# Kernel optimization log

Hardware: AMD Instinct MI355X
Metric: run time of the kernel (lower is better)

The kernel has to match this reference:

```python
import jax, jax.numpy as jnp
import numpy as np
from jax import lax

H = 2048      # d_inner
N = 8         # half of d_state (conjugate-pair complex modes)
B, L, D_MODEL = 4, 4096, 1024
D_CONV = 4


def setup_inputs() -> dict:
    key = jax.random.key(0)
    ks = jax.random.split(key, 10)
    hidden_states = jax.random.normal(ks[0], (B, L, D_MODEL), dtype=jnp.float32)
    W_in = jax.random.normal(ks[1], (2 * H, D_MODEL), dtype=jnp.float32) / np.sqrt(D_MODEL)
    conv_w = jax.random.normal(ks[2], (H, D_CONV), dtype=jnp.float32) / np.sqrt(D_CONV)
    conv_b = jax.random.normal(ks[3], (H,), dtype=jnp.float32) * 0.1
    # S4D params: dt ~ loguniform(1e-3, 1e-1); A = -0.5 + i*pi*n (legs-ish diag init)
    u = jax.random.uniform(ks[4], (H,), dtype=jnp.float32)
    log_dt = jnp.log(1e-3) + u * (jnp.log(1e-1) - jnp.log(1e-3))
    log_A_real = jnp.log(0.5 * jnp.ones((H, N), dtype=jnp.float32))
    A_imag = jnp.pi * jnp.broadcast_to(jnp.arange(N, dtype=jnp.float32), (H, N)).copy()
    C_re = jax.random.normal(ks[5], (H, N), dtype=jnp.float32)
    C_im = jax.random.normal(ks[6], (H, N), dtype=jnp.float32)
    D = jnp.ones((H,), dtype=jnp.float32)
    W_out = jax.random.normal(ks[7], (D_MODEL, H), dtype=jnp.float32) / np.sqrt(H)
    return dict(hidden_states=hidden_states, W_in=W_in, conv_w=conv_w, conv_b=conv_b,
                log_dt=log_dt, log_A_real=log_A_real, A_imag=A_imag,
                C_re=C_re, C_im=C_im, D=D, W_out=W_out)


def _s4d_kernel(log_dt, log_A_real, A_imag, C_re, C_im, L):
    # S4D (diagonal SSM) convolution kernel, ZOH-style discretization.
    dt = jnp.exp(log_dt)                       # (H,)
    A = -jnp.exp(log_A_real) + 1j * A_imag      # (H,N) complex
    C = C_re + 1j * C_im                        # (H,N)
    dtA = dt[:, None] * A                       # (H,N)
    Ct = C * (jnp.exp(dtA) - 1.0) / A           # (H,N)
    t = jnp.arange(L, dtype=jnp.float32)
    vand = jnp.exp(dtA[:, :, None] * t)         # (H,N,L) Vandermonde
    return 2.0 * jnp.einsum('hn,hnl->hl', Ct, vand).real  # (H,L)


def reference(hidden_states, W_in, conv_w, conv_b, log_dt, log_A_real, A_imag, C_re, C_im, D, W_out):
    B, L, _ = hidden_states.shape
    # in_proj (no bias): (B,L,D) -> (B, 2H, L)
    xz = jnp.einsum('bld,ed->bel', hidden_states, W_in)
    x, z = jnp.split(xz, 2, axis=1)             # each (B,H,L)
    # causal depthwise conv1d + SiLU
    w = conv_w.shape[-1]
    xp = jnp.pad(x, ((0, 0), (0, 0), (w - 1, 0)))
    x = lax.conv_general_dilated(xp, conv_w[:, None, :], (1,), 'VALID',
                                 dimension_numbers=('NCH', 'OIH', 'NCH'),
                                 feature_group_count=x.shape[1])
    x = jax.nn.silu(x + conv_b[None, :, None])
    # S4 FFT long convolution + D skip
    k = _s4d_kernel(log_dt, log_A_real, A_imag, C_re, C_im, L)  # (H,L)
    n = 2 * L
    y = jnp.fft.irfft(jnp.fft.rfft(x, n=n) * jnp.fft.rfft(k, n=n), n=n)[..., :L]
    y = y + x * D[None, :, None]
    # SiLU gate and out_proj
    y = y * jax.nn.silu(z)
    return jnp.einsum('bhl,dh->bld', y, W_out)
```

## Files before the change

kernel.cpp:

```cpp
#include <hip/hip_runtime.h>
#include <hip/hip_bf16.h>
#include <math.h>

#define H_DIM 2048
#define N_ST 8
#define B_SZ 4
#define L_SEQ 4096
#define DMODEL 1024
#define DCONV 4
#define CL 128
#define NC (L_SEQ / CL)

typedef __bf16 bf16x8 __attribute__((ext_vector_type(8)));
typedef __bf16 bf16x4 __attribute__((ext_vector_type(4)));
typedef float f32x4 __attribute__((ext_vector_type(4)));

typedef const unsigned int __attribute__((address_space(1)))* gptr_t;
typedef unsigned int __attribute__((address_space(3)))* lptr_t;

__device__ __forceinline__ void gl_lds16(const __bf16* g, __bf16* l) {
    __builtin_amdgcn_global_load_lds((gptr_t)g, (lptr_t)l, 16, 0, 0);
}

#define WS_XZ     0
#define WS_YTH    8388608
#define WS_YTL    12582912
#define WS_COEF   16777216
#define WS_STATES 16875520
#define WS_LOOK   17924096
#define WS_HH     18186240
#define WS_HL     20283392
#define WS_WIH    22380544
#define WS_WIL    24477696
#define WS_WOH    26574848
#define WS_WOL    27623424

__global__ __launch_bounds__(256) void cvt_split4(const float* __restrict__ s,
                                                  __bf16* __restrict__ h,
                                                  __bf16* __restrict__ l, int n4) {
    int i = blockIdx.x * 256 + threadIdx.x;
    if (i >= n4) return;
    float4 v = ((const float4*)s)[i];
    float vv[4] = {v.x, v.y, v.z, v.w};
    bf16x4 hv, lv;
#pragma unroll
    for (int j = 0; j < 4; ++j) {
        __bf16 hb = (__bf16)vv[j];
        hv[j] = hb;
        lv[j] = (__bf16)(vv[j] - (float)hb);
    }
    *(bf16x4*)&h[(size_t)i * 4] = hv;
    *(bf16x4*)&l[(size_t)i * 4] = lv;
}

__global__ void coef_kernel(const float* __restrict__ log_dt,
                            const float* __restrict__ log_A_real,
                            const float* __restrict__ A_imag,
                            const float* __restrict__ C_re,
                            const float* __restrict__ C_im,
                            float* __restrict__ coef) {
    int i = blockIdx.x * blockDim.x + threadIdx.x;
    if (i >= H_DIM * N_ST) return;
    int h = i >> 3;
    float dt = expf(log_dt[h]);
    float Ar = -expf(log_A_real[i]);
    float Ai = A_imag[i];
    float er = expf(dt * Ar);
    float ang = dt * Ai;
    float wr = er * cosf(ang);
    float wi = er * sinf(ang);
    float den = Ar * Ar + Ai * Ai;
    float qr = ((wr - 1.f) * Ar + wi * Ai) / den;
    float qi = (wi * Ar - (wr - 1.f) * Ai) / den;
    float Cr = C_re[i], Ci = C_im[i];
    float Ctr = Cr * qr - Ci * qi;
    float Cti = Cr * qi + Ci * qr;
    float eCL = expf((float)CL * dt * Ar);
    float aCL = (float)CL * dt * Ai;
    float pr = eCL * cosf(aCL);
    float pi = eCL * sinf(aCL);
    const int HN = H_DIM * N_ST;
    coef[i]          = wr;
    coef[HN + i]     = wi;
    coef[2 * HN + i] = Ctr;
    coef[3 * HN + i] = Cti;
    coef[4 * HN + i] = pr;
    coef[5 * HN + i] = pi;
}

__global__ __launch_bounds__(256, 2) void gemm_split(const __bf16* __restrict__ Ah,
                                                     const __bf16* __restrict__ Al,
                                                     const __bf16* __restrict__ Bh,
                                                     const __bf16* __restrict__ Bl,
                                                     float* __restrict__ C,
                                                     int K, int ldc) {
    __shared__ __bf16 sAh[2][4096], sAl[2][4096], sBh[2][4096], sBl[2][4096];
    const int tid = threadIdx.x;
    const int lane = tid & 63;
    const int wid = tid >> 6;
    const int wrw = wid >> 1, wcw = wid & 1;
    const int bm = blockIdx.y, bn = blockIdx.x;

    const int r = tid & 127;
    const int kbq8 = (tid >> 7) * 8;
    const size_t arow = (size_t)(bm * 128 + r) * K;
    const size_t brow = (size_t)(bn * 128 + r) * K;

    f32x4 acc[4][4];
#pragma unroll
    for (int m = 0; m < 4; ++m)
#pragma unroll
        for (int n = 0; n < 4; ++n) acc[m][n] = (f32x4){0.f, 0.f, 0.f, 0.f};

    const int kb = lane >> 4, rr = lane & 15;

    auto stage = [&](int b, int k0) {
#pragma unroll
        for (int q = 0; q < 2; ++q) {
            const int lo = q * 2048 + tid * 8;
            const size_t go = (size_t)k0 + q * 16 + kbq8;
            gl_lds16(Ah + arow + go, &sAh[b][lo]);
            gl_lds16(Al + arow + go, &sAl[b][lo]);
            gl_lds16(Bh + brow + go, &sBh[b][lo]);
            gl_lds16(Bl + brow + go, &sBl[b][lo]);
        }
    };

    const int nt = K >> 5;
    stage(0, 0);
    stage(1, 32);
    asm volatile("s_waitcnt vmcnt(8)" ::: "memory");
    __builtin_amdgcn_s_barrier();

    for (int t = 0; t < nt; ++t) {
        const int cur = t & 1;

        bf16x8 fAh[4], fAl[4], fBh[4], fBl[4];
#pragma unroll
        for (int m = 0; m < 4; ++m) {
            int off = kb * 1024 + (wrw * 64 + m * 16 + rr) * 8;
            fAh[m] = *(const bf16x8*)&sAh[cur][off];
            fAl[m] = *(const bf16x8*)&sAl[cur][off];
        }
#pragma unroll
        for (int n = 0; n < 4; ++n) {
            int off = kb * 1024 + (wcw * 64 + n * 16 + rr) * 8;
            fBh[n] = *(const bf16x8*)&sBh[cur][off];
            fBl[n] = *(const bf16x8*)&sBl[cur][off];
        }
        asm volatile("s_waitcnt lgkmcnt(0)" ::: "memory");
        __builtin_amdgcn_sched_barrier(0);
        __builtin_amdgcn_s_barrier();
        __builtin_amdgcn_sched_barrier(0);
        if (t + 2 < nt) stage(cur, (t + 2) << 5);
        __builtin_amdgcn_s_setprio(1);
#pragma unroll
        for (int m = 0; m < 4; ++m)
#pragma unroll
            for (int n = 0; n < 4; ++n) {
                acc[m][n] = __builtin_amdgcn_mfma_f32_16x16x32_bf16(fAh[m], fBh[n], acc[m][n], 0, 0, 0);
                acc[m][n] = __builtin_amdgcn_mfma_f32_16x16x32_bf16(fAh[m], fBl[n], acc[m][n], 0, 0, 0);
                acc[m][n] = __builtin_amdgcn_mfma_f32_16x16x32_bf16(fAl[m], fBh[n], acc[m][n], 0, 0, 0);
            }
        __builtin_amdgcn_s_setprio(0);
        if (t + 2 < nt) asm volatile("s_waitcnt vmcnt(8)" ::: "memory");
        else            asm volatile("s_waitcnt vmcnt(0)" ::: "memory");
        __builtin_amdgcn_s_barrier();
    }

    const int rq = lane >> 4;
#pragma unroll
    for (int m = 0; m < 4; ++m)
#pragma unroll
        for (int n = 0; n < 4; ++n) {
            int col = bn * 128 + wcw * 64 + n * 16 + rr;
            int row0 = bm * 128 + wrw * 64 + m * 16 + rq * 4;
#pragma unroll
            for (int j = 0; j < 4; ++j)
                C[(size_t)(row0 + j) * ldc + col] = acc[m][n][j];
        }
}

__global__ __launch_bounds__(256) void scan_phase1(const float* __restrict__ xz,
                                                   const float* __restrict__ coef,
                                                   const float* __restrict__ conv_w,
                                                   const float* __restrict__ conv_b,
                                                   float* __restrict__ states,
                                                   float* __restrict__ look) {
    int t = blockIdx.x * 256 + threadIdx.x;
    int c = t & (NC - 1);
    int h = t >> 5;

    const int HN = H_DIM * N_ST;
    float wr[N_ST], wi[N_ST];
#pragma unroll
    for (int n = 0; n < N_ST; ++n) {
        wr[n] = coef[h * N_ST + n];
        wi[n] = coef[HN + h * N_ST + n];
    }
    float cw0 = conv_w[h * 4 + 0], cw1 = conv_w[h * 4 + 1];
    float cw2 = conv_w[h * 4 + 2], cw3 = conv_w[h * 4 + 3];
    float cb = conv_b[h];

    const float* xrow = xz + (size_t)h * L_SEQ + c * CL;
    float x3 = 0.f, x2 = 0.f, x1 = 0.f;
    if (c > 0) {
        float4 p = *(const float4*)(xrow - 4);
        x3 = p.y; x2 = p.z; x1 = p.w;
    }
    *(float4*)(look + (size_t)t * 4) = make_float4(x3, x2, x1, 0.f);

    float sr[N_ST], si[N_ST];
#pragma unroll
    for (int n = 0; n < N_ST; ++n) { sr[n] = 0.f; si[n] = 0.f; }

    for (int j = 0; j < CL; j += 4) {
        float4 v = *(const float4*)(xrow + j);
        float xv[4] = {v.x, v.y, v.z, v.w};
#pragma unroll
        for (int k = 0; k < 4; ++k) {
            float u = cw0 * x3 + cw1 * x2 + cw2 * x1 + cw3 * xv[k] + cb;
            float xc = u / (1.f + __expf(-u));
            x3 = x2; x2 = x1; x1 = xv[k];
#pragma unroll
            for (int n = 0; n < N_ST; ++n) {
                float nr = wr[n] * sr[n] - wi[n] * si[n] + xc;
                float ni = wr[n] * si[n] + wi[n] * sr[n];
                sr[n] = nr; si[n] = ni;
            }
        }
    }
    float* st = states + (size_t)t * (N_ST * 2);
#pragma unroll
    for (int n = 0; n < N_ST; ++n) { st[2 * n] = sr[n]; st[2 * n + 1] = si[n]; }
}

__global__ __launch_bounds__(256) void scan_phase2(const float* __restrict__ coef,
                                                   float* __restrict__ states) {
    int h = blockIdx.x * 256 + threadIdx.x;
    if (h >= H_DIM) return;
    const int HN = H_DIM * N_ST;
    float pr[N_ST], pi[N_ST];
#pragma unroll
    for (int n = 0; n < N_ST; ++n) {
        pr[n] = coef[4 * HN + h * N_ST + n];
        pi[n] = coef[5 * HN + h * N_ST + n];
    }
    float sr[N_ST], si[N_ST];
#pragma unroll
    for (int n = 0; n < N_ST; ++n) { sr[n] = 0.f; si[n] = 0.f; }
    float* base = states + (size_t)h * NC * (N_ST * 2);
    for (int c = 0; c < NC; ++c) {
        float* st = base + c * (N_ST * 2);
#pragma unroll
        for (int n = 0; n < N_ST; ++n) {
            float lr = st[2 * n], li = st[2 * n + 1];
            st[2 * n] = sr[n]; st[2 * n + 1] = si[n];
            float nr = pr[n] * sr[n] - pi[n] * si[n] + lr;
            float ni = pr[n] * si[n] + pi[n] * sr[n] + li;
            sr[n] = nr; si[n] = ni;
        }
    }
}

__global__ __launch_bounds__(256) void scan_phase3(float* __restrict__ xz,
                                                   const float* __restrict__ coef,
                                                   const float* __restrict__ conv_w,
                                                   const float* __restrict__ conv_b,
                                                   const float* __restrict__ Dvec,
                                                   const float* __restrict__ states,
                                                   const float* __restrict__ look) {
    int t = blockIdx.x * 256 + threadIdx.x;
    int c = t & (NC - 1);
    int h = t >> 5;

    const int HN = H_DIM * N_ST;
    float wr[N_ST], wi[N_ST], Ctr[N_ST], Cti[N_ST];
#pragma unroll
    for (int n = 0; n < N_ST; ++n) {
        wr[n]  = coef[h * N_ST + n];
        wi[n]  = coef[HN + h * N_ST + n];
        Ctr[n] = coef[2 * HN + h * N_ST + n];
        Cti[n] = coef[3 * HN + h * N_ST + n];
    }
    float cw0 = conv_w[h * 4 + 0], cw1 = conv_w[h * 4 + 1];
    float cw2 = conv_w[h * 4 + 2], cw3 = conv_w[h * 4 + 3];
    float cb = conv_b[h];
    float Dh = Dvec[h];

    float* xrow = xz + (size_t)h * L_SEQ + c * CL;
    const float* zrow = xz + (size_t)(H_DIM + h) * L_SEQ + c * CL;

    float4 lk = *(const float4*)(look + (size_t)t * 4);
    float x3 = lk.x, x2 = lk.y, x1 = lk.z;

    const float* st = states + (size_t)t * (N_ST * 2);
    float sr[N_ST], si[N_ST];
#pragma unroll
    for (int n = 0; n < N_ST; ++n) { sr[n] = st[2 * n]; si[n] = st[2 * n + 1]; }

    for (int j = 0; j < CL; j += 4) {
        float4 v = *(const float4*)(xrow + j);
        float4 zv = *(const float4*)(zrow + j);
        float xv[4] = {v.x, v.y, v.z, v.w};
        float zz[4] = {zv.x, zv.y, zv.z, zv.w};
        float out[4];
#pragma unroll
        for (int k = 0; k < 4; ++k) {
            float u = cw0 * x3 + cw1 * x2 + cw2 * x1 + cw3 * xv[k] + cb;
            float xc = u / (1.f + __expf(-u));
            x3 = x2; x2 = x1; x1 = xv[k];
            float accy = 0.f;
#pragma unroll
            for (int n = 0; n < N_ST; ++n) {
                float nr = wr[n] * sr[n] - wi[n] * si[n] + xc;
                float ni = wr[n] * si[n] + wi[n] * sr[n];
                sr[n] = nr; si[n] = ni;
                accy += Ctr[n] * nr - Cti[n] * ni;
            }
            float yv = 2.f * accy + Dh * xc;
            float g = zz[k] / (1.f + __expf(-zz[k]));
            out[k] = yv * g;
        }
        *(float4*)(xrow + j) = make_float4(out[0], out[1], out[2], out[3]);
    }
}

__global__ __launch_bounds__(256) void transpose_split(const float* __restrict__ y,
                                                       __bf16* __restrict__ th,
                                                       __bf16* __restrict__ tl) {
    __shared__ float tile[64][65];
    const int l0 = blockIdx.x * 64, h0 = blockIdx.y * 64;
    const int tid = threadIdx.x;
    const int r = tid >> 4, c4 = (tid & 15) * 4;
#pragma unroll
    for (int p = 0; p < 4; ++p) {
        float4 v = *(const float4*)(y + (size_t)(h0 + r + p * 16) * L_SEQ + l0 + c4);
        tile[r + p * 16][c4 + 0] = v.x;
        tile[r + p * 16][c4 + 1] = v.y;
        tile[r + p * 16][c4 + 2] = v.z;
        tile[r + p * 16][c4 + 3] = v.w;
    }
    __syncthreads();
    const int l = tid >> 2, hb = (tid & 3) * 16;
    float vals[16];
#pragma unroll
    for (int j = 0; j < 16; ++j) vals[j] = tile[hb + j][l];
    bf16x8 hv0, hv1, lv0, lv1;
#pragma unroll
    for (int j = 0; j < 8; ++j) {
        __bf16 hbv = (__bf16)vals[j];
        hv0[j] = hbv;
        lv0[j] = (__bf16)(vals[j] - (float)hbv);
        __bf16 hbv2 = (__bf16)vals[j + 8];
        hv1[j] = hbv2;
        lv1[j] = (__bf16)(vals[j + 8] - (float)hbv2);
    }
    size_t base = (size_t)(l0 + l) * H_DIM + h0 + hb;
    *(bf16x8*)&th[base] = hv0;
    *(bf16x8*)&th[base + 8] = hv1;
    *(bf16x8*)&tl[base] = lv0;
    *(bf16x8*)&tl[base + 8] = lv1;
}

extern "C" void kernel_launch(void* const* d_in, const int* in_sizes, int n_in,
                              void* d_out, int out_size, void* d_ws, size_t ws_size,
                              hipStream_t stream) {
    const float* hid        = (const float*)d_in[0];
    const float* W_in       = (const float*)d_in[1];
    const float* conv_w     = (const float*)d_in[2];
    const float* conv_b     = (const float*)d_in[3];
    const float* log_dt     = (const float*)d_in[4];
    const float* log_A_real = (const float*)d_in[5];
    const float* A_imag     = (const float*)d_in[6];
    const float* C_re       = (const float*)d_in[7];
    const float* C_im       = (const float*)d_in[8];
    const float* Dv         = (const float*)d_in[9];
    const float* W_out      = (const float*)d_in[10];
    float* out = (float*)d_out;
    float* ws  = (float*)d_ws;

    float* xz      = ws + WS_XZ;
    __bf16* yTh    = (__bf16*)(ws + WS_YTH);
    __bf16* yTl    = (__bf16*)(ws + WS_YTL);
    float* coef    = ws + WS_COEF;
    float* states  = ws + WS_STATES;
    float* look    = ws + WS_LOOK;
    __bf16* Hh     = (__bf16*)(ws + WS_HH);
    __bf16* Hl     = (__bf16*)(ws + WS_HL);
    __bf16* Wih    = (__bf16*)(ws + WS_WIH);
    __bf16* Wil    = (__bf16*)(ws + WS_WIL);
    __bf16* Woh    = (__bf16*)(ws + WS_WOH);
    __bf16* Wol    = (__bf16*)(ws + WS_WOL);

    coef_kernel<<<(H_DIM * N_ST + 255) / 256, 256, 0, stream>>>(
        log_dt, log_A_real, A_imag, C_re, C_im, coef);

    cvt_split4<<<(2 * H_DIM * DMODEL / 4 + 255) / 256, 256, 0, stream>>>(W_in, Wih, Wil, 2 * H_DIM * DMODEL / 4);
    cvt_split4<<<(DMODEL * H_DIM / 4 + 255) / 256, 256, 0, stream>>>(W_out, Woh, Wol, DMODEL * H_DIM / 4);

    const int nscan = H_DIM * NC;
    dim3 gIn(L_SEQ / 128, 2 * H_DIM / 128);
    dim3 gOut(DMODEL / 128, L_SEQ / 128);
    dim3 gTr(L_SEQ / 64, H_DIM / 64);

    for (int b = 0; b < B_SZ; ++b) {
        const float* hid_b = hid + (size_t)b * L_SEQ * DMODEL;
        float* out_b = out + (size_t)b * L_SEQ * DMODEL;

        cvt_split4<<<(L_SEQ * DMODEL / 4 + 255) / 256, 256, 0, stream>>>(hid_b, Hh, Hl, L_SEQ * DMODEL / 4);
        gemm_split<<<gIn, 256, 0, stream>>>(Wih, Wil, Hh, Hl, xz, DMODEL, L_SEQ);
        scan_phase1<<<nscan / 256, 256, 0, stream>>>(xz, coef, conv_w, conv_b, states, look);
        scan_phase2<<<(H_DIM + 255) / 256, 256, 0, stream>>>(coef, states);
        scan_phase3<<<nscan / 256, 256, 0, stream>>>(xz, coef, conv_w, conv_b, Dv, states, look);
        transpose_split<<<gTr, 256, 0, stream>>>(xz, yTh, yTl);
        gemm_split<<<gOut, 256, 0, stream>>>(yTh, yTl, Woh, Wol, out_b, H_DIM, DMODEL);
    }
}
```

Measured before the change: 1.632 ms.

## Add 256x256-tile split-bf16 GEMM with interleaved prefetch for in_proj

Adds a 512-thread GEMM kernel with 256x256 output tiles, 8 waves each computing a 128x64 sub-tile with the three-term bf16 split (hi*hi, hi*lo, lo*hi). LDS fragment loads for A are split in two phases, and the next k-tile's global-to-LDS copies are issued in two halves interleaved with the MFMA groups, which run under raised wave priority. The in_proj GEMM uses this kernel, aiming for more operand reuse per LDS byte and better overlap of loads with matrix math. The costs are much higher register pressure (128 accumulator floats per thread), 128 KB of LDS per block, and only 64 blocks for the in_proj GEMM, which may underfill the GPU.

```diff
diff --git a/kernel.cpp b/kernel.cpp
--- a/kernel.cpp
+++ b/kernel.cpp
@@ -88,6 +88,138 @@
     coef[5 * HN + i] = pi;
 }
 
+__global__ __launch_bounds__(512, 2) void gemm_split256(const __bf16* __restrict__ Ah,
+                                                        const __bf16* __restrict__ Al,
+                                                        const __bf16* __restrict__ Bh,
+                                                        const __bf16* __restrict__ Bl,
+                                                        float* __restrict__ C,
+                                                        int K, int ldc) {
+    __shared__ __bf16 sAh[2][8192], sAl[2][8192], sBh[2][8192], sBl[2][8192];
+    const int tid = threadIdx.x;
+    const int lane = tid & 63;
+    const int wid = tid >> 6;
+    const int wrw = wid >> 2;
+    const int wcw = wid & 3;
+    const int bm = blockIdx.y, bn = blockIdx.x;
+
+    const int srow = tid & 255;
+    const int skb0 = tid >> 8;
+    const size_t aGrow = (size_t)(bm * 256 + srow) * K;
+    const size_t bGrow = (size_t)(bn * 256 + srow) * K;
+
+    f32x4 acc[8][4];
+#pragma unroll
+    for (int m = 0; m < 8; ++m)
+#pragma unroll
+        for (int n = 0; n < 4; ++n) acc[m][n] = (f32x4){0.f, 0.f, 0.f, 0.f};
+
+    const int kb = lane >> 4, rr = lane & 15;
+    const int offA0 = kb * 2048 + (wrw * 128 + rr) * 8;
+    const int offB0 = kb * 2048 + (wcw * 64 + rr) * 8;
+
+    auto stage_half = [&](int b, int k0, int q) {
+        const int lo = q * 4096 + tid * 8;
+        const size_t go = (size_t)k0 + (size_t)((skb0 + 2 * q) * 8);
+        gl_lds16(Ah + aGrow + go, &sAh[b][lo]);
+        gl_lds16(Al + aGrow + go, &sAl[b][lo]);
+        gl_lds16(Bh + bGrow + go, &sBh[b][lo]);
+        gl_lds16(Bl + bGrow + go, &sBl[b][lo]);
+    };
+
+    const int nt = K >> 5;
+    stage_half(0, 0, 0);  stage_half(0, 0, 1);
+    stage_half(1, 32, 0); stage_half(1, 32, 1);
+    asm volatile("s_waitcnt vmcnt(8)" ::: "memory");
+    __builtin_amdgcn_s_barrier();
+
+    for (int t = 0; t < nt; ++t) {
+        const int cur = t & 1;
+        const __bf16* pAh = sAh[cur];
+        const __bf16* pAl = sAl[cur];
+        const __bf16* pBh = sBh[cur];
+        const __bf16* pBl = sBl[cur];
+
+        bf16x8 fBh[4], fBl[4], fAh8[8], fAl8[8];
+#pragma unroll
+        for (int n = 0; n < 4; ++n) {
+            fBh[n] = *(const bf16x8*)&pBh[offB0 + n * 128];
+            fBl[n] = *(const bf16x8*)&pBl[offB0 + n * 128];
+        }
+#pragma unroll
+        for (int m = 0; m < 2; ++m) {
+            fAh8[m] = *(const bf16x8*)&pAh[offA0 + m * 128];
+            fAl8[m] = *(const bf16x8*)&pAl[offA0 + m * 128];
+        }
+        asm volatile("s_waitcnt lgkmcnt(0)" ::: "memory");
+        __builtin_amdgcn_sched_barrier(0);
+        __builtin_amdgcn_s_setprio(1);
+#pragma unroll
+        for (int m = 0; m < 2; ++m)
+#pragma unroll
+            for (int n = 0; n < 4; ++n) {
+                acc[m][n] = __builtin_amdgcn_mfma_f32_16x16x32_bf16(fAh8[m], fBh[n], acc[m][n], 0, 0, 0);
+                acc[m][n] = __builtin_amdgcn_mfma_f32_16x16x32_bf16(fAh8[m], fBl[n], acc[m][n], 0, 0, 0);
+                acc[m][n] = __builtin_amdgcn_mfma_f32_16x16x32_bf16(fAl8[m], fBh[n], acc[m][n], 0, 0, 0);
+            }
+        __builtin_amdgcn_s_setprio(0);
+#pragma unroll
+        for (int m = 2; m < 8; ++m) {
+            fAh8[m] = *(const bf16x8*)&pAh[offA0 + m * 128];
+            fAl8[m] = *(const bf16x8*)&pAl[offA0 + m * 128];
+        }
+        asm volatile("s_waitcnt lgkmcnt(0)" ::: "memory");
+        __builtin_amdgcn_sched_barrier(0);
+        __builtin_amdgcn_s_setprio(1);
+#pragma unroll
+        for (int m = 2; m < 4; ++m)
+#pragma unroll
+            for (int n = 0; n < 4; ++n) {
+                acc[m][n] = __builtin_amdgcn_mfma_f32_16x16x32_bf16(fAh8[m], fBh[n], acc[m][n], 0, 0, 0);
+                acc[m][n] = __builtin_amdgcn_mfma_f32_16x16x32_bf16(fAh8[m], fBl[n], acc[m][n], 0, 0, 0);
+                acc[m][n] = __builtin_amdgcn_mfma_f32_16x16x32_bf16(fAl8[m], fBh[n], acc[m][n], 0, 0, 0);
+            }
+        __builtin_amdgcn_s_setprio(0);
+        __builtin_amdgcn_s_barrier();
+        if (t + 2 < nt) stage_half(cur, (t + 2) << 5, 0);
+        __builtin_amdgcn_s_setprio(1);
+#pragma unroll
+        for (int m = 4; m < 6; ++m)
+#pragma unroll
+            for (int n = 0; n < 4; ++n) {
+                acc[m][n] = __builtin_amdgcn_mfma_f32_16x16x32_bf16(fAh8[m], fBh[n], acc[m][n], 0, 0, 0);
+                acc[m][n] = __builtin_amdgcn_mfma_f32_16x16x32_bf16(fAh8[m], fBl[n], acc[m][n], 0, 0, 0);
+                acc[m][n] = __builtin_amdgcn_mfma_f32_16x16x32_bf16(fAl8[m], fBh[n], acc[m][n], 0, 0, 0);
+            }
+        __builtin_amdgcn_s_setprio(0);
+        if (t + 2 < nt) stage_half(cur, (t + 2) << 5, 1);
+        __builtin_amdgcn_s_setprio(1);
+#pragma unroll
+        for (int m = 6; m < 8; ++m)
+#pragma unroll
+            for (int n = 0; n < 4; ++n) {
+                acc[m][n] = __builtin_amdgcn_mfma_f32_16x16x32_bf16(fAh8[m], fBh[n], acc[m][n], 0, 0, 0);
+                acc[m][n] = __builtin_amdgcn_mfma_f32_16x16x32_bf16(fAh8[m], fBl[n], acc[m][n], 0, 0, 0);
+                acc[m][n] = __builtin_amdgcn_mfma_f32_16x16x32_bf16(fAl8[m], fBh[n], acc[m][n], 0, 0, 0);
+            }
+        __builtin_amdgcn_s_setprio(0);
+        if (t + 2 < nt) asm volatile("s_waitcnt vmcnt(8)" ::: "memory");
+        else            asm volatile("s_waitcnt vmcnt(0)" ::: "memory");
+        __builtin_amdgcn_s_barrier();
+    }
+
+    const int rq = lane >> 4;
+#pragma unroll
+    for (int m = 0; m < 8; ++m)
+#pragma unroll
+        for (int n = 0; n < 4; ++n) {
+            int col = bn * 256 + wcw * 64 + n * 16 + rr;
+            int row0 = bm * 256 + wrw * 128 + m * 16 + rq * 4;
+#pragma unroll
+            for (int j = 0; j < 4; ++j)
+                C[(size_t)(row0 + j) * ldc + col] = acc[m][n][j];
+        }
+}
+
 __global__ __launch_bounds__(256, 2) void gemm_split(const __bf16* __restrict__ Ah,
                                                      const __bf16* __restrict__ Al,
                                                      const __bf16* __restrict__ Bh,
@@ -134,7 +266,6 @@
 
     for (int t = 0; t < nt; ++t) {
         const int cur = t & 1;
-
         bf16x8 fAh[4], fAl[4], fBh[4], fBl[4];
 #pragma unroll
         for (int m = 0; m < 4; ++m) {
@@ -400,7 +531,7 @@
     cvt_split4<<<(DMODEL * H_DIM / 4 + 255) / 256, 256, 0, stream>>>(W_out, Woh, Wol, DMODEL * H_DIM / 4);
 
     const int nscan = H_DIM * NC;
-    dim3 gIn(L_SEQ / 128, 2 * H_DIM / 128);
+    dim3 gIn2(L_SEQ / 256, 2 * H_DIM / 256);
     dim3 gOut(DMODEL / 128, L_SEQ / 128);
     dim3 gTr(L_SEQ / 64, H_DIM / 64);
 
@@ -409,7 +540,7 @@
         float* out_b = out + (size_t)b * L_SEQ * DMODEL;
 
         cvt_split4<<<(L_SEQ * DMODEL / 4 + 255) / 256, 256, 0, stream>>>(hid_b, Hh, Hl, L_SEQ * DMODEL / 4);
-        gemm_split<<<gIn, 256, 0, stream>>>(Wih, Wil, Hh, Hl, xz, DMODEL, L_SEQ);
+        gemm_split256<<<gIn2, 512, 0, stream>>>(Wih, Wil, Hh, Hl, xz, DMODEL, L_SEQ);
         scan_phase1<<<nscan / 256, 256, 0, stream>>>(xz, coef, conv_w, conv_b, states, look);
         scan_phase2<<<(H_DIM + 255) / 256, 256, 0, stream>>>(coef, states);
         scan_phase3<<<nscan / 256, 256, 0, stream>>>(xz, coef, conv_w, conv_b, Dv, states, look);
```

Result: no change. 1.603 ms (-1.8%).

## Fuse bf16 hi/lo split into tripled-K layout with 256x256 GEMM tile

Applied to the files above, without the earlier changes.

The in_proj GEMM now uses a new data layout in which each 8-element k-chunk is stored as [hi,hi,lo] for the weights and [hi,lo,hi] for the activations. One plain bf16 GEMM over K=3072 then produces the three split-precision products (hi*hi, hi*lo, lo*hi). The new kernel uses 512 threads, a 256x256 output tile, a 4-stage global-to-LDS pipeline and setprio around the MFMA blocks. The aim is to raise data reuse and MFMA density and to cut the separate hi/lo LDS traffic. The cost is a larger activation workspace and more register and LDS pressure.

```diff
diff --git a/kernel.cpp b/kernel.cpp
--- a/kernel.cpp
+++ b/kernel.cpp
@@ -28,12 +28,10 @@
 #define WS_COEF   16777216
 #define WS_STATES 16875520
 #define WS_LOOK   17924096
-#define WS_HH     18186240
-#define WS_HL     20283392
-#define WS_WIH    22380544
-#define WS_WIL    24477696
-#define WS_WOH    26574848
-#define WS_WOL    27623424
+#define WS_HF     18186240
+#define WS_WIF    24477696
+#define WS_WOH    30769152
+#define WS_WOL    31817728
 
 __global__ __launch_bounds__(256) void cvt_split4(const float* __restrict__ s,
                                                   __bf16* __restrict__ h,
@@ -51,6 +49,31 @@
     }
     *(bf16x4*)&h[(size_t)i * 4] = hv;
     *(bf16x4*)&l[(size_t)i * 4] = lv;
+}
+
+template <int BSIDE>
+__global__ __launch_bounds__(256) void cvt_fuse(const float* __restrict__ s,
+                                                __bf16* __restrict__ d, int nOct) {
+    int i = blockIdx.x * 256 + threadIdx.x;
+    if (i >= nOct) return;
+    int row = i >> 7, ko = i & 127;
+    const float* p = s + (size_t)row * 1024 + ko * 8;
+    float4 v0 = *(const float4*)p;
+    float4 v1 = *(const float4*)(p + 4);
+    float vv[8] = {v0.x, v0.y, v0.z, v0.w, v1.x, v1.y, v1.z, v1.w};
+    bf16x8 hv, lv;
+#pragma unroll
+    for (int j = 0; j < 8; ++j) {
+        __bf16 hb = (__bf16)vv[j];
+        hv[j] = hb;
+        lv[j] = (__bf16)(vv[j] - (float)hb);
+    }
+    __bf16* o = d + (size_t)row * 3072 + ko * 24;
+    if (BSIDE) {
+        *(bf16x8*)(o) = hv; *(bf16x8*)(o + 8) = lv; *(bf16x8*)(o + 16) = hv;
+    } else {
+        *(bf16x8*)(o) = hv; *(bf16x8*)(o + 8) = hv; *(bf16x8*)(o + 16) = lv;
+    }
 }
 
 __global__ void coef_kernel(const float* __restrict__ log_dt,
@@ -88,6 +111,101 @@
     coef[5 * HN + i] = pi;
 }
 
+__global__ __launch_bounds__(512, 2) void gemm_fused256(const __bf16* __restrict__ A,
+                                                        const __bf16* __restrict__ B,
+                                                        float* __restrict__ C,
+                                                        int K, int ldc) {
+    __shared__ __bf16 sA[4][8192], sB[4][8192];
+    const int tid = threadIdx.x;
+    const int lane = tid & 63;
+    const int wid = tid >> 6;
+    const int wrw = wid >> 2, wcw = wid & 3;
+    const int bm = blockIdx.y, bn = blockIdx.x;
+
+    f32x4 acc[8][4];
+#pragma unroll
+    for (int m = 0; m < 8; ++m)
+#pragma unroll
+        for (int n = 0; n < 4; ++n) acc[m][n] = (f32x4){0.f, 0.f, 0.f, 0.f};
+
+    const int kb = lane >> 4, rr = lane & 15;
+    const int offA0 = kb * 2048 + (wrw * 128 + rr) * 8;
+    const int offB0 = kb * 2048 + (wcw * 64 + rr) * 8;
+
+    auto stage_pair = [&](int t, int l) {
+        const int buf = t & 3;
+        const int L = l * 512 + tid;
+        const int ko = L >> 8, row = L & 255;
+        const size_t goff = (size_t)t * 32 + ko * 8;
+        gl_lds16(A + (size_t)(bm * 256 + row) * K + goff, &sA[buf][L * 8]);
+        gl_lds16(B + (size_t)(bn * 256 + row) * K + goff, &sB[buf][L * 8]);
+    };
+
+    const int nt = K >> 5;
+    stage_pair(0, 0); stage_pair(0, 1);
+    stage_pair(1, 0); stage_pair(1, 1);
+    stage_pair(2, 0); stage_pair(2, 1);
+    asm volatile("s_waitcnt vmcnt(8)" ::: "memory");
+    __builtin_amdgcn_sched_barrier(0);
+    __builtin_amdgcn_s_barrier();
+
+#pragma unroll 1
+    for (int t = 0; t < nt; ++t) {
+        const int buf = t & 3;
+        const __bf16* pA = sA[buf];
+        const __bf16* pB = sB[buf];
+        bf16x8 fB[4], fA[8];
+
+#pragma unroll
+        for (int n = 0; n < 4; ++n) fB[n] = *(const bf16x8*)&pB[offB0 + n * 128];
+#pragma unroll
+        for (int m = 0; m < 4; ++m) fA[m] = *(const bf16x8*)&pA[offA0 + m * 128];
+        if (t + 3 < nt) stage_pair(t + 3, 0);
+        __builtin_amdgcn_s_barrier();
+        asm volatile("s_waitcnt lgkmcnt(0)" ::: "memory");
+        __builtin_amdgcn_sched_barrier(0);
+        __builtin_amdgcn_s_setprio(1);
+#pragma unroll
+        for (int m = 0; m < 4; ++m)
+#pragma unroll
+            for (int n = 0; n < 4; ++n)
+                acc[m][n] = __builtin_amdgcn_mfma_f32_16x16x32_bf16(fA[m], fB[n], acc[m][n], 0, 0, 0);
+        __builtin_amdgcn_s_setprio(0);
+        __builtin_amdgcn_s_barrier();
+
+#pragma unroll
+        for (int m = 4; m < 8; ++m) fA[m] = *(const bf16x8*)&pA[offA0 + m * 128];
+        if (t + 3 < nt) stage_pair(t + 3, 1);
+        __builtin_amdgcn_s_barrier();
+        asm volatile("s_waitcnt lgkmcnt(0)" ::: "memory");
+        __builtin_amdgcn_sched_barrier(0);
+        __builtin_amdgcn_s_setprio(1);
+#pragma unroll
+        for (int m = 4; m < 8; ++m)
+#pragma unroll
+            for (int n = 0; n < 4; ++n)
+                acc[m][n] = __builtin_amdgcn_mfma_f32_16x16x32_bf16(fA[m], fB[n], acc[m][n], 0, 0, 0);
+        __builtin_amdgcn_s_setprio(0);
+        if (t + 3 < nt)      asm volatile("s_waitcnt vmcnt(8)" ::: "memory");
+        else if (t + 2 < nt) asm volatile("s_waitcnt vmcnt(4)" ::: "memory");
+        else                 asm volatile("s_waitcnt vmcnt(0)" ::: "memory");
+        __builtin_amdgcn_sched_barrier(0);
+        __builtin_amdgcn_s_barrier();
+    }
+
+    const int rq = lane >> 4;
+#pragma unroll
+    for (int m = 0; m < 8; ++m)
+#pragma unroll
+        for (int n = 0; n < 4; ++n) {
+            int col = bn * 256 + wcw * 64 + n * 16 + rr;
+            int row0 = bm * 256 + wrw * 128 + m * 16 + rq * 4;
+#pragma unroll
+            for (int j = 0; j < 4; ++j)
+                C[(size_t)(row0 + j) * ldc + col] = acc[m][n][j];
+        }
+}
+
 __global__ __launch_bounds__(256, 2) void gemm_split(const __bf16* __restrict__ Ah,
                                                      const __bf16* __restrict__ Al,
                                                      const __bf16* __restrict__ Bh,
@@ -134,7 +252,6 @@
 
     for (int t = 0; t < nt; ++t) {
         const int cur = t & 1;
-
         bf16x8 fAh[4], fAl[4], fBh[4], fBl[4];
 #pragma unroll
         for (int m = 0; m < 4; ++m) {
@@ -386,21 +503,21 @@
     float* coef    = ws + WS_COEF;
     float* states  = ws + WS_STATES;
     float* look    = ws + WS_LOOK;
-    __bf16* Hh     = (__bf16*)(ws + WS_HH);
-    __bf16* Hl     = (__bf16*)(ws + WS_HL);
-    __bf16* Wih    = (__bf16*)(ws + WS_WIH);
-    __bf16* Wil    = (__bf16*)(ws + WS_WIL);
+    __bf16* Hf     = (__bf16*)(ws + WS_HF);
+    __bf16* WiF    = (__bf16*)(ws + WS_WIF);
     __bf16* Woh    = (__bf16*)(ws + WS_WOH);
     __bf16* Wol    = (__bf16*)(ws + WS_WOL);
 
     coef_kernel<<<(H_DIM * N_ST + 255) / 256, 256, 0, stream>>>(
         log_dt, log_A_real, A_imag, C_re, C_im, coef);
 
-    cvt_split4<<<(2 * H_DIM * DMODEL / 4 + 255) / 256, 256, 0, stream>>>(W_in, Wih, Wil, 2 * H_DIM * DMODEL / 4);
+    const int wOct = 2 * H_DIM * DMODEL / 8;
+    cvt_fuse<0><<<(wOct + 255) / 256, 256, 0, stream>>>(W_in, WiF, wOct);
     cvt_split4<<<(DMODEL * H_DIM / 4 + 255) / 256, 256, 0, stream>>>(W_out, Woh, Wol, DMODEL * H_DIM / 4);
 
     const int nscan = H_DIM * NC;
-    dim3 gIn(L_SEQ / 128, 2 * H_DIM / 128);
+    const int hOct = L_SEQ * DMODEL / 8;
+    dim3 gIn(L_SEQ / 256, 2 * H_DIM / 256);
     dim3 gOut(DMODEL / 128, L_SEQ / 128);
     dim3 gTr(L_SEQ / 64, H_DIM / 64);
 
@@ -408,8 +525,8 @@
         const float* hid_b = hid + (size_t)b * L_SEQ * DMODEL;
         float* out_b = out + (size_t)b * L_SEQ * DMODEL;
 
-        cvt_split4<<<(L_SEQ * DMODEL / 4 + 255) / 256, 256, 0, stream>>>(hid_b, Hh, Hl, L_SEQ * DMODEL / 4);
-        gemm_split<<<gIn, 256, 0, stream>>>(Wih, Wil, Hh, Hl, xz, DMODEL, L_SEQ);
+        cvt_fuse<1><<<(hOct + 255) / 256, 256, 0, stream>>>(hid_b, Hf, hOct);
+        gemm_fused256<<<gIn, 512, 0, stream>>>(WiF, Hf, xz, 3 * DMODEL, L_SEQ);
         scan_phase1<<<nscan / 256, 256, 0, stream>>>(xz, coef, conv_w, conv_b, states, look);
         scan_phase2<<<(H_DIM + 255) / 256, 256, 0, stream>>>(coef, states);
         scan_phase3<<<nscan / 256, 256, 0, stream>>>(xz, coef, conv_w, conv_b, Dv, states, look);
```

New measurement: 1.853 ms. +13.6%, slower.
